# Performance work log

Hardware: AMD Instinct MI355X
Metric: run time of the kernel (lower is better)

Reference implementation:

```python
import jax, jax.numpy as jnp
import numpy as np
import math

B, S, D, NH, L = 4, 1024, 512, 8, 2
PRED, COUT = 96, 512
DH = D // NH
EPS_BACKEND = 1e-6
EPS_LN = 1e-5


def setup_inputs() -> dict:
    key = jax.random.key(0)
    ks = jax.random.split(key, 8)
    return {
        "x_enc": jax.random.normal(ks[0], (B, S, D), jnp.float32),
        "x_mark_enc": jax.random.normal(ks[1], (B, S, 4), jnp.float32),
        "x_dec": jax.random.normal(ks[2], (B, PRED, D), jnp.float32),
        "x_mark_dec": jax.random.normal(ks[3], (B, PRED, 4), jnp.float32),
        # per-layer mLSTM cell params (stacked over L layers)
        "W_ig": jax.random.normal(ks[4], (L, NH, 3 * D), jnp.float32) * 0.02,
        "b_ig": jnp.zeros((L, NH), jnp.float32),
        "W_fg": jax.random.normal(ks[5], (L, NH, 3 * D), jnp.float32) * 0.02,
        "b_fg": jnp.zeros((L, NH), jnp.float32),
        "ln_w": jnp.ones((L, D), jnp.float32),
        # final head
        "fc_W": jax.random.normal(ks[6], (COUT, D), jnp.float32) * 0.02,
        "fc_b": jnp.zeros((COUT,), jnp.float32),
    }


def _mlstm_cell(q, k, v, W_ig, b_ig, W_fg, b_fg, ln_w):
    """xlstm parallel_stabilized_simple backend + MultiHeadLayerNorm."""
    Bq, Sq, Dq = q.shape
    gate_in = jnp.concatenate([q, k, v], axis=-1)          # [B,S,3D]
    ig = jnp.einsum('bsd,hd->bhs', gate_in, W_ig) + b_ig[None, :, None]  # [B,NH,S]
    fg = jnp.einsum('bsd,hd->bhs', gate_in, W_fg) + b_fg[None, :, None]  # [B,NH,S]

    qh = q.reshape(Bq, Sq, NH, DH).transpose(0, 2, 1, 3)   # [B,NH,S,DH]
    kh = k.reshape(Bq, Sq, NH, DH).transpose(0, 2, 1, 3)
    vh = v.reshape(Bq, Sq, NH, DH).transpose(0, 2, 1, 3)

    log_f = jax.nn.log_sigmoid(fg)                          # [B,NH,S]
    fcum = jnp.cumsum(log_f, axis=-1)                       # F[i] = sum_{t<=i} log_f[t]
    # log_fg_matrix[i,j] = F[i] - F[j] for j<=i, else -inf
    lfg = fcum[..., :, None] - fcum[..., None, :]           # [B,NH,S,S]
    causal = jnp.tril(jnp.ones((Sq, Sq), dtype=bool))
    log_D = jnp.where(causal, lfg + ig[..., None, :], -jnp.inf)  # [B,NH,S,S]

    max_log_D = jnp.max(log_D, axis=-1, keepdims=True)      # row-wise stabilizer
    Dm = jnp.exp(log_D - max_log_D)

    qk = jnp.einsum('bhsd,bhtd->bhst', qh, kh) * (1.0 / math.sqrt(DH))
    C = qk * Dm
    normalizer = jnp.maximum(jnp.abs(jnp.sum(C, axis=-1, keepdims=True)),
                             jnp.exp(-max_log_D))
    Cn = C / (normalizer + EPS_BACKEND)
    h = jnp.einsum('bhst,bhtd->bhsd', Cn, vh)               # [B,NH,S,DH]

    # MultiHeadLayerNorm == GroupNorm over DH per head, weight only (no bias)
    mu = jnp.mean(h, axis=-1, keepdims=True)
    var = jnp.var(h, axis=-1, keepdims=True)
    hn = (h - mu) * jax.lax.rsqrt(var + EPS_LN)
    hn = hn * ln_w.reshape(NH, DH)[None, :, None, :]
    return hn.transpose(0, 2, 1, 3).reshape(Bq, Sq, Dq)     # [B,S,D]


def reference(x_enc, x_mark_enc, x_dec, x_mark_dec,
              W_ig, b_ig, W_fg, b_fg, ln_w, fc_W, fc_b):
    q = x_enc
    k = x_enc
    v = x_enc
    for l in range(L):
        q = _mlstm_cell(q, k, v, W_ig[l], b_ig[l], W_fg[l], b_fg[l], ln_w[l])
    dec_out = jnp.einsum('bsd,od->bso', q[:, -PRED:, :], fc_W) + fc_b
    return dec_out
```

## Files before the change

### kernel.cpp

```cpp
#include <hip/hip_runtime.h>
#include <hip/hip_bf16.h>
#include <math.h>
#include <stdint.h>

#define B_ 4
#define S_ 1024
#define D_ 512
#define NH_ 8
#define DH_ 64
#define L_ 2
#define PRED_ 96
#define COUT_ 512

typedef __attribute__((ext_vector_type(8))) short short8;
typedef __attribute__((ext_vector_type(4))) float f32x4;

__device__ __forceinline__ unsigned short f2bf(float f) {
  union { float f; unsigned int u; } v; v.f = f;
  unsigned int r = v.u + 0x7fffu + ((v.u >> 16) & 1u);
  return (unsigned short)(r >> 16);
}
__device__ __forceinline__ float bf2f(unsigned short h) {
  union { unsigned int u; float f; } v; v.u = (unsigned int)h << 16;
  return v.f;
}

__global__ __launch_bounds__(64) void convkv_kernel(
    const float* __restrict__ x, unsigned short* __restrict__ hiA,
    unsigned short* __restrict__ loA) {
  int bs = blockIdx.x;
  int b = bs >> 10, s = bs & 1023;
  int t = threadIdx.x;
  int h = t >> 3, dh0 = (t & 7) * 8;
  const float* src = x + (size_t)bs * D_ + t * 8;
  float4 v0 = *(const float4*)(src);
  float4 v1 = *(const float4*)(src + 4);
  float xv[8] = {v0.x, v0.y, v0.z, v0.w, v1.x, v1.y, v1.z, v1.w};
  unsigned short hh[8], ll[8];
#pragma unroll
  for (int k = 0; k < 8; ++k) {
    hh[k] = f2bf(xv[k]);
    ll[k] = f2bf(xv[k] - bf2f(hh[k]));
  }
  size_t off = (((size_t)(b * NH_ + h)) * S_ + s) * 64 + dh0;
  *(uint4*)(hiA + off) = *(const uint4*)hh;
  *(uint4*)(loA + off) = *(const uint4*)ll;
}

__global__ __launch_bounds__(256) void transpose_kernel(
    const unsigned short* __restrict__ src_a, unsigned short* __restrict__ dst_a) {
  int jt = blockIdx.x, h = blockIdx.y, b = blockIdx.z;
  int bh = b * NH_ + h, j0 = jt * 64;
  __shared__ unsigned short tile[64][72];
  int t = threadIdx.x;
  {
    int j = t >> 2, dseg = (t & 3) * 16;
    const unsigned short* src = src_a + ((size_t)bh * S_ + j0 + j) * 64 + dseg;
    uint4 a0 = *(const uint4*)(src);
    uint4 a1 = *(const uint4*)(src + 8);
    *(uint4*)(&tile[j][dseg]) = a0;
    *(uint4*)(&tile[j][dseg + 8]) = a1;
  }
  __syncthreads();
  {
    int d = t >> 2, jseg = (t & 3) * 16;
    unsigned short us[16];
#pragma unroll
    for (int k = 0; k < 16; ++k) us[k] = tile[jseg + k][d];
    unsigned short* dst = dst_a + ((size_t)bh * 64 + d) * S_ + j0 + jseg;
    *(uint4*)(dst) = *(const uint4*)us;
    *(uint4*)(dst + 8) = *(const uint4*)(us + 8);
  }
}

__global__ __launch_bounds__(256) void gates2_kernel(
    const float* __restrict__ q, const float* __restrict__ x,
    const float* __restrict__ Wig, const float* __restrict__ big,
    const float* __restrict__ Wfg, const float* __restrict__ bfg,
    float* __restrict__ ig_out, float* __restrict__ fg_out) {
  int sc = blockIdx.x, hg = blockIdx.y, b = blockIdx.z;
  __shared__ float Wq_s[8][512];
  __shared__ float Wc_s[8][512];
  for (int idx = threadIdx.x; idx < 8 * 512; idx += 256) {
    int p = idx >> 9, e = idx & 511;
    int h = hg * 4 + (p >> 1);
    const float* Wr = ((p & 1) ? Wfg : Wig) + (size_t)h * (3 * D_);
    Wq_s[p][e] = Wr[e];
    Wc_s[p][e] = Wr[512 + e] + Wr[1024 + e];
  }
  __syncthreads();
  int wv = threadIdx.x >> 6, l = threadIdx.x & 63;
  for (int rr = 0; rr < 8; ++rr) {
    int s = sc * 32 + wv * 8 + rr;
    const float* qrow = q + ((size_t)(b * S_ + s)) * D_;
    const float* xrow = x + ((size_t)(b * S_ + s)) * D_;
    float ql[8], xl[8];
#pragma unroll
    for (int k = 0; k < 8; ++k) { ql[k] = qrow[l + 64 * k]; xl[k] = xrow[l + 64 * k]; }
#pragma unroll
    for (int p = 0; p < 8; ++p) {
      float acc = 0.f;
#pragma unroll
      for (int k = 0; k < 8; ++k)
        acc += Wq_s[p][l + 64 * k] * ql[k] + Wc_s[p][l + 64 * k] * xl[k];
#pragma unroll
      for (int off = 32; off; off >>= 1) acc += __shfl_down(acc, off);
      if (l == 0) {
        int h = hg * 4 + (p >> 1);
        float v = acc + ((p & 1) ? bfg : big)[h];
        ((p & 1) ? fg_out : ig_out)[((size_t)(b * NH_ + h)) * S_ + s] = v;
      }
    }
  }
}

__global__ __launch_bounds__(64) void scan_kernel(
    const float* __restrict__ ig, const float* __restrict__ fg,
    float* __restrict__ a_out, float* __restrict__ amax_out) {
  int bh = blockIdx.x;
  int lane = threadIdx.x;
  const float* igr = ig + (size_t)bh * S_;
  const float* fgr = fg + (size_t)bh * S_;
  const int CH = S_ / 64;
  float lf[16], av[16];
  float lsum = 0.f;
  int base = lane * CH;
  for (int u = 0; u < CH; ++u) {
    float xv = fgr[base + u];
    float ls = (xv >= 0.f) ? -log1pf(__expf(-xv)) : (xv - log1pf(__expf(xv)));
    lf[u] = ls; lsum += ls;
  }
  float pref = lsum;
#pragma unroll
  for (int off = 1; off < 64; off <<= 1) {
    float t = __shfl_up(pref, off);
    if (lane >= off) pref += t;
  }
  float F = pref - lsum;
  float lamax = -INFINITY;
  for (int u = 0; u < CH; ++u) {
    F += lf[u];
    float a = igr[base + u] - F;
    av[u] = a;
    lamax = fmaxf(lamax, a);
  }
  float pmax = lamax;
#pragma unroll
  for (int off = 1; off < 64; off <<= 1) {
    float t = __shfl_up(pmax, off);
    if (lane >= off) pmax = fmaxf(pmax, t);
  }
  float run = __shfl_up(pmax, 1);
  if (lane == 0) run = -INFINITY;
  for (int u = 0; u < CH; ++u) {
    run = fmaxf(run, av[u]);
    size_t o = (size_t)bh * S_ + base + u;
    a_out[o] = av[u];
    amax_out[o] = run;
  }
}

__global__ __launch_bounds__(256) void attn_mfma_kernel(
    const float* __restrict__ qin,
    const unsigned short* __restrict__ kH, const unsigned short* __restrict__ kL,
    const unsigned short* __restrict__ tH, const unsigned short* __restrict__ tL,
    const float* __restrict__ a_arr, const float* __restrict__ amax_arr,
    const float* __restrict__ lnw, float* __restrict__ out,
    unsigned short* __restrict__ outH, unsigned short* __restrict__ outL,
    int write_bf, int it0, int orow0, int out_srows) {
  int it = blockIdx.x + it0, h = blockIdx.y, b = blockIdx.z;
  int i0 = it * 64;
  int bh = b * NH_ + h;
  int tid = threadIdx.x;
  int w = tid >> 6, l = tid & 63;
  int l15 = l & 15, lg = l >> 4;

  __shared__ __align__(16) unsigned char smem[49152 + 256];
  unsigned char* KsH = smem;
  unsigned char* KsL = smem + 8192;
  unsigned char* VtH = smem + 16384;
  unsigned char* VtL = smem + 24576;
  unsigned char* PwH = smem + 32768 + w * 2048;
  unsigned char* PwL = smem + 40960 + w * 2048;
  float* aLds = (float*)(smem + 49152);

  short8 qh[2], qlo[2];
  {
    const float* qrow = qin + ((size_t)(b * S_ + i0 + w * 16 + l15)) * D_ + h * DH_;
#pragma unroll
    for (int ks = 0; ks < 2; ++ks) {
      const float* p = qrow + ks * 32 + lg * 8;
      float4 v0 = *(const float4*)(p);
      float4 v1 = *(const float4*)(p + 4);
      float xv[8] = {v0.x, v0.y, v0.z, v0.w, v1.x, v1.y, v1.z, v1.w};
      unsigned short hh[8], ll[8];
#pragma unroll
      for (int k = 0; k < 8; ++k) {
        hh[k] = f2bf(xv[k]);
        ll[k] = f2bf(xv[k] - bf2f(hh[k]));
      }
      qh[ks] = *(const short8*)hh;
      qlo[ks] = *(const short8*)ll;
    }
  }
  float am_i = amax_arr[(size_t)bh * S_ + i0 + w * 16 + l15];
  const float* abase = a_arr + (size_t)bh * S_;

  f32x4 acc[4];
#pragma unroll
  for (int nt = 0; nt < 4; ++nt) acc[nt] = (f32x4){0.f, 0.f, 0.f, 0.f};

  const unsigned short* KsrcH = kH + (size_t)bh * S_ * 64;
  const unsigned short* KsrcL = kL + (size_t)bh * S_ * 64;
  const unsigned short* TsrcH = tH + (size_t)bh * 64 * S_;
  const unsigned short* TsrcL = tL + (size_t)bh * 64 * S_;

  for (int jt = 0; jt <= it; ++jt) {
    int j0 = jt * 64;
    __syncthreads();
    {
      int r = w * 16 + l15;
#pragma unroll
      for (int gb = 0; gb < 8; gb += 4) {
        int g = gb + lg;
        int sw = r * 128 + ((g ^ (r & 7)) * 16);
        *(uint4*)(KsH + sw) = *(const uint4*)(KsrcH + ((size_t)(j0 + r)) * 64 + g * 8);
        *(uint4*)(KsL + sw) = *(const uint4*)(KsrcL + ((size_t)(j0 + r)) * 64 + g * 8);
        *(uint4*)(VtH + sw) = *(const uint4*)(TsrcH + (size_t)r * S_ + j0 + g * 8);
        *(uint4*)(VtL + sw) = *(const uint4*)(TsrcL + (size_t)r * S_ + j0 + g * 8);
      }
    }
    if (tid < 64) aLds[tid] = abase[j0 + tid];
    __syncthreads();
    int i_g = i0 + w * 16 + l15;
#pragma unroll
    for (int js = 0; js < 4; ++js) {
      f32x4 st = (f32x4){0.f, 0.f, 0.f, 0.f};
      int krow = js * 16 + l15;
      int key = krow & 7;
      short8 kh0 = *(const short8*)(KsH + krow * 128 + (((0 + lg) ^ key) * 16));
      short8 kh1 = *(const short8*)(KsH + krow * 128 + (((4 + lg) ^ key) * 16));
      short8 kl0 = *(const short8*)(KsL + krow * 128 + (((0 + lg) ^ key) * 16));
      short8 kl1 = *(const short8*)(KsL + krow * 128 + (((4 + lg) ^ key) * 16));
      st = __builtin_amdgcn_mfma_f32_16x16x32_bf16(kh0, qh[0], st, 0, 0, 0);
      st = __builtin_amdgcn_mfma_f32_16x16x32_bf16(kh1, qh[1], st, 0, 0, 0);
      st = __builtin_amdgcn_mfma_f32_16x16x32_bf16(kh0, qlo[0], st, 0, 0, 0);
      st = __builtin_amdgcn_mfma_f32_16x16x32_bf16(kh1, qlo[1], st, 0, 0, 0);
      st = __builtin_amdgcn_mfma_f32_16x16x32_bf16(kl0, qh[0], st, 0, 0, 0);
      st = __builtin_amdgcn_mfma_f32_16x16x32_bf16(kl1, qh[1], st, 0, 0, 0);
      int jb_loc = js * 16 + lg * 4;
      unsigned int pkh[2], pkl[2];
#pragma unroll
      for (int r2 = 0; r2 < 2; ++r2) {
        unsigned int ph = 0, pl = 0;
#pragma unroll
        for (int rr = 0; rr < 2; ++rr) {
          int r = r2 * 2 + rr;
          int jl = jb_loc + r;
          float e = __expf(fminf(aLds[jl] - am_i, 0.f));
          float wv = (j0 + jl <= i_g) ? st[r] * 0.125f * e : 0.f;
          unsigned short whi = f2bf(wv);
          unsigned short wlo = f2bf(wv - bf2f(whi));
          ph |= (unsigned int)whi << (rr * 16);
          pl |= (unsigned int)wlo << (rr * 16);
        }
        pkh[r2] = ph; pkl[r2] = pl;
      }
      int g = js * 2 + (lg >> 1);
      int pw_off = l15 * 128 + ((g ^ (l15 & 7)) * 16) + (lg & 1) * 8;
      *(uint2*)(PwH + pw_off) = make_uint2(pkh[0], pkh[1]);
      *(uint2*)(PwL + pw_off) = make_uint2(pkl[0], pkl[1]);
    }
#pragma unroll
    for (int ks = 0; ks < 2; ++ks) {
      int pg = ((ks * 4 + lg) ^ (l15 & 7)) * 16;
      short8 ph = *(const short8*)(PwH + l15 * 128 + pg);
      short8 pl = *(const short8*)(PwL + l15 * 128 + pg);
#pragma unroll
      for (int nt = 0; nt < 4; ++nt) {
        int vr = nt * 16 + l15;
        int vg = vr * 128 + (((ks * 4 + lg) ^ (vr & 7)) * 16);
        short8 vh = *(const short8*)(VtH + vg);
        short8 vl = *(const short8*)(VtL + vg);
        acc[nt] = __builtin_amdgcn_mfma_f32_16x16x32_bf16(ph, vh, acc[nt], 0, 0, 0);
        acc[nt] = __builtin_amdgcn_mfma_f32_16x16x32_bf16(pl, vh, acc[nt], 0, 0, 0);
        acc[nt] = __builtin_amdgcn_mfma_f32_16x16x32_bf16(ph, vl, acc[nt], 0, 0, 0);
      }
    }
  }

  float lw[4];
#pragma unroll
  for (int nt = 0; nt < 4; ++nt) lw[nt] = lnw[h * DH_ + nt * 16 + l15];
#pragma unroll
  for (int r = 0; r < 4; ++r) {
    int il = lg * 4 + r;
    int i_glob = i0 + w * 16 + il;
    float hv[4], s1 = 0.f, s2 = 0.f;
#pragma unroll
    for (int nt = 0; nt < 4; ++nt) {
      hv[nt] = acc[nt][r];
      s1 += hv[nt]; s2 += hv[nt] * hv[nt];
    }
#pragma unroll
    for (int off = 1; off < 16; off <<= 1) {
      s1 += __shfl_xor(s1, off); s2 += __shfl_xor(s2, off);
    }
    float mean = s1 * (1.f / 64.f);
    float var = s2 * (1.f / 64.f) - mean * mean;
    float rstd = rsqrtf(var + 1e-5f);
    size_t ro = ((size_t)(b * out_srows + (i_glob - orow0))) * D_ + h * DH_;
    if (!write_bf) {
#pragma unroll
      for (int nt = 0; nt < 4; ++nt)
        out[ro + nt * 16 + l15] = (hv[nt] - mean) * rstd * lw[nt];
    } else {
#pragma unroll
      for (int nt = 0; nt < 4; ++nt) {
        float v = (hv[nt] - mean) * rstd * lw[nt];
        unsigned short hi = f2bf(v);
        outH[ro + nt * 16 + l15] = hi;
        outL[ro + nt * 16 + l15] = f2bf(v - bf2f(hi));
      }
    }
  }
}

__global__ __launch_bounds__(256) void fc3_kernel(
    const unsigned short* __restrict__ qH, const unsigned short* __restrict__ qL,
    const float* __restrict__ W, const float* __restrict__ bias,
    float* __restrict__ out) {
  int rt = blockIdx.x, ot = blockIdx.y;
  int tid = threadIdx.x;
  int w = tid >> 6, l = tid & 63, l15 = l & 15, lg = l >> 4;
  int r_flat = rt * 64 + w * 16 + l15;
  int b = r_flat / 96, pc = r_flat - b * 96;
  const unsigned short* qHrow = qH + ((size_t)(b * 128 + 32 + pc)) * D_;
  const unsigned short* qLrow = qL + ((size_t)(b * 128 + 32 + pc)) * D_;
  int obase = ot * 64;

  f32x4 acc[4];
#pragma unroll
  for (int og = 0; og < 4; ++og) acc[og] = (f32x4){0.f, 0.f, 0.f, 0.f};

#pragma unroll 2
  for (int ks = 0; ks < 16; ++ks) {
    int k0 = ks * 32 + lg * 8;
    short8 ah = *(const short8*)(qHrow + k0);
    short8 al = *(const short8*)(qLrow + k0);
#pragma unroll
    for (int og = 0; og < 4; ++og) {
      const float* wrow = W + (size_t)(obase + og * 16 + l15) * D_ + k0;
      float4 w0 = *(const float4*)(wrow);
      float4 w1 = *(const float4*)(wrow + 4);
      float wv[8] = {w0.x, w0.y, w0.z, w0.w, w1.x, w1.y, w1.z, w1.w};
      unsigned short bhh[8], bll[8];
#pragma unroll
      for (int k = 0; k < 8; ++k) {
        bhh[k] = f2bf(wv[k]);
        bll[k] = f2bf(wv[k] - bf2f(bhh[k]));
      }
      short8 bh = *(const short8*)bhh;
      short8 bl = *(const short8*)bll;
      acc[og] = __builtin_amdgcn_mfma_f32_16x16x32_bf16(ah, bh, acc[og], 0, 0, 0);
      acc[og] = __builtin_amdgcn_mfma_f32_16x16x32_bf16(al, bh, acc[og], 0, 0, 0);
      acc[og] = __builtin_amdgcn_mfma_f32_16x16x32_bf16(ah, bl, acc[og], 0, 0, 0);
    }
  }
  int rbase = rt * 64 + w * 16 + lg * 4;
#pragma unroll
  for (int og = 0; og < 4; ++og) {
    int o = obase + og * 16 + l15;
    float bs = bias[o];
#pragma unroll
    for (int r = 0; r < 4; ++r)
      out[(size_t)(rbase + r) * COUT_ + o] = acc[og][r] + bs;
  }
}

extern "C" void kernel_launch(void* const* d_in, const int* in_sizes, int n_in,
                              void* d_out, int out_size, void* d_ws, size_t ws_size,
                              hipStream_t stream) {
  const float* x_enc = (const float*)d_in[0];
  const float* W_ig = (const float*)d_in[4];
  const float* b_ig = (const float*)d_in[5];
  const float* W_fg = (const float*)d_in[6];
  const float* b_fg = (const float*)d_in[7];
  const float* ln_w = (const float*)d_in[8];
  const float* fc_W = (const float*)d_in[9];
  const float* fc_b = (const float*)d_in[10];

  float* ws = (float*)d_ws;
  const size_t NBSD = (size_t)B_ * S_ * D_;
  const size_t NBHS = (size_t)B_ * NH_ * S_;
  float* h1 = ws;
  float* ig = h1 + NBSD;
  float* fg = ig + NBHS;
  float* aA = fg + NBHS;
  float* amaxA = aA + NBHS;
  unsigned short* kvhH = (unsigned short*)(amaxA + NBHS);
  unsigned short* kvhL = kvhH + NBSD;
  unsigned short* kvTH = kvhL + NBSD;
  unsigned short* kvTL = kvTH + NBSD;
  unsigned short* hqH = kvTL + NBSD;
  unsigned short* hqL = hqH + (size_t)B_ * 128 * D_;

  convkv_kernel<<<B_ * S_, 64, 0, stream>>>(x_enc, kvhH, kvhL);
  transpose_kernel<<<dim3(S_ / 64, NH_, B_), 256, 0, stream>>>(kvhH, kvTH);
  transpose_kernel<<<dim3(S_ / 64, NH_, B_), 256, 0, stream>>>(kvhL, kvTL);

  for (int l = 0; l < L_; ++l) {
    const float* qin = (l == 0) ? x_enc : h1;
    gates2_kernel<<<dim3(S_ / 32, 2, B_), 256, 0, stream>>>(
        qin, x_enc,
        W_ig + (size_t)l * NH_ * 3 * D_, b_ig + (size_t)l * NH_,
        W_fg + (size_t)l * NH_ * 3 * D_, b_fg + (size_t)l * NH_, ig, fg);
    scan_kernel<<<B_ * NH_, 64, 0, stream>>>(ig, fg, aA, amaxA);
    if (l == 0) {
      attn_mfma_kernel<<<dim3(S_ / 64, NH_, B_), 256, 0, stream>>>(
          qin, kvhH, kvhL, kvTH, kvTL, aA, amaxA, ln_w + (size_t)l * D_,
          h1, (unsigned short*)nullptr, (unsigned short*)nullptr, 0, 0, 0, S_);
    } else {
      attn_mfma_kernel<<<dim3(2, NH_, B_), 256, 0, stream>>>(
          qin, kvhH, kvhL, kvTH, kvTL, aA, amaxA, ln_w + (size_t)l * D_,
          (float*)nullptr, hqH, hqL, 1, 14, 896, 128);
    }
  }
  fc3_kernel<<<dim3(6, 8), 256, 0, stream>>>(hqH, hqL, fc_W, fc_b, (float*)d_out);
}
```

Baseline: 299.0 us.

## Give each wave its own 16-row tile, pair causal tiles, read K/V from global

The attention kernel is restructured so each wavefront independently owns a 16-row query tile, and in layer 0 processes a complementary pair (t and 63-t) to balance causal work. K and V tiles are no longer staged in shared LDS with block barriers; each wave loads its MFMA operands straight from global memory and relies on the cache. Block-to-(b,h) mapping is permuted so blocks sharing a head land on the same XCD for L2 reuse. This removes __syncthreads and the causal load imbalance, at the cost of more global/cache traffic and less data sharing across waves.

```diff
diff --git a/kernel.cpp b/kernel.cpp
--- a/kernel.cpp
+++ b/kernel.cpp
@@ -160,169 +160,182 @@
   }
 }
 
-__global__ __launch_bounds__(256) void attn_mfma_kernel(
+__device__ __forceinline__ void attn_tile_proc(
+    int t, int b, int h, int bh, int l15, int lg,
+    const float* __restrict__ qin,
+    const unsigned short* __restrict__ KsrcH, const unsigned short* __restrict__ KsrcL,
+    const unsigned short* __restrict__ TsrcH, const unsigned short* __restrict__ TsrcL,
+    const float* __restrict__ abase, const float* __restrict__ amax_arr,
+    const float* __restrict__ lnw,
+    float* __restrict__ out, unsigned short* __restrict__ outH,
+    unsigned short* __restrict__ outL,
+    int write_bf, int orow0, int out_srows,
+    unsigned char* PwH, unsigned char* PwL) {
+  int i0 = t * 16;
+  short8 qh[2], qlo[2];
+  {
+    const float* qrow = qin + ((size_t)(b * S_ + i0 + l15)) * D_ + h * DH_;
+#pragma unroll
+    for (int ks = 0; ks < 2; ++ks) {
+      const float* p = qrow + ks * 32 + lg * 8;
+      float4 v0 = *(const float4*)(p);
+      float4 v1 = *(const float4*)(p + 4);
+      float xv[8] = {v0.x, v0.y, v0.z, v0.w, v1.x, v1.y, v1.z, v1.w};
+      unsigned short hh[8], ll[8];
+#pragma unroll
+      for (int k = 0; k < 8; ++k) {
+        hh[k] = f2bf(xv[k]);
+        ll[k] = f2bf(xv[k] - bf2f(hh[k]));
+      }
+      qh[ks] = *(const short8*)hh;
+      qlo[ks] = *(const short8*)ll;
+    }
+  }
+  float am_i = amax_arr[(size_t)bh * S_ + i0 + l15];
+  int i_g = i0 + l15;
+  f32x4 acc[4];
+#pragma unroll
+  for (int nt = 0; nt < 4; ++nt) acc[nt] = (f32x4){0.f, 0.f, 0.f, 0.f};
+
+  int jt_max = (i0 + 15) >> 6;
+  for (int jt = 0; jt <= jt_max; ++jt) {
+    int j0 = jt * 64;
+#pragma unroll
+    for (int js = 0; js < 4; ++js) {
+      int jr = j0 + js * 16 + l15;
+      const unsigned short* kp = KsrcH + (size_t)jr * 64 + lg * 8;
+      const unsigned short* kpl = KsrcL + (size_t)jr * 64 + lg * 8;
+      short8 kh0 = *(const short8*)(kp);
+      short8 kh1 = *(const short8*)(kp + 32);
+      short8 kl0 = *(const short8*)(kpl);
+      short8 kl1 = *(const short8*)(kpl + 32);
+      f32x4 st = (f32x4){0.f, 0.f, 0.f, 0.f};
+      st = __builtin_amdgcn_mfma_f32_16x16x32_bf16(kh0, qh[0], st, 0, 0, 0);
+      st = __builtin_amdgcn_mfma_f32_16x16x32_bf16(kh1, qh[1], st, 0, 0, 0);
+      st = __builtin_amdgcn_mfma_f32_16x16x32_bf16(kh0, qlo[0], st, 0, 0, 0);
+      st = __builtin_amdgcn_mfma_f32_16x16x32_bf16(kh1, qlo[1], st, 0, 0, 0);
+      st = __builtin_amdgcn_mfma_f32_16x16x32_bf16(kl0, qh[0], st, 0, 0, 0);
+      st = __builtin_amdgcn_mfma_f32_16x16x32_bf16(kl1, qh[1], st, 0, 0, 0);
+      int jb = js * 16 + lg * 4;
+      unsigned int pkh[2], pkl[2];
+#pragma unroll
+      for (int r2 = 0; r2 < 2; ++r2) {
+        unsigned int ph = 0, pl = 0;
+#pragma unroll
+        for (int rr = 0; rr < 2; ++rr) {
+          int r = r2 * 2 + rr;
+          int jl = jb + r;
+          float e = __expf(fminf(abase[j0 + jl] - am_i, 0.f));
+          float wv = (j0 + jl <= i_g) ? st[r] * 0.125f * e : 0.f;
+          unsigned short whi = f2bf(wv);
+          ph |= (unsigned int)whi << (rr * 16);
+          pl |= (unsigned int)f2bf(wv - bf2f(whi)) << (rr * 16);
+        }
+        pkh[r2] = ph; pkl[r2] = pl;
+      }
+      int g = js * 2 + (lg >> 1);
+      int pw_off = l15 * 128 + ((g ^ (l15 & 7)) * 16) + (lg & 1) * 8;
+      *(uint2*)(PwH + pw_off) = make_uint2(pkh[0], pkh[1]);
+      *(uint2*)(PwL + pw_off) = make_uint2(pkl[0], pkl[1]);
+    }
+#pragma unroll
+    for (int ks = 0; ks < 2; ++ks) {
+      int pg = ((ks * 4 + lg) ^ (l15 & 7)) * 16;
+      short8 ph = *(const short8*)(PwH + l15 * 128 + pg);
+      short8 pl = *(const short8*)(PwL + l15 * 128 + pg);
+#pragma unroll
+      for (int nt = 0; nt < 4; ++nt) {
+        const unsigned short* vp = TsrcH + (size_t)(nt * 16 + l15) * S_ + j0 + (ks * 4 + lg) * 8;
+        const unsigned short* vpl = TsrcL + (size_t)(nt * 16 + l15) * S_ + j0 + (ks * 4 + lg) * 8;
+        short8 vh = *(const short8*)vp;
+        short8 vl = *(const short8*)vpl;
+        acc[nt] = __builtin_amdgcn_mfma_f32_16x16x32_bf16(ph, vh, acc[nt], 0, 0, 0);
+        acc[nt] = __builtin_amdgcn_mfma_f32_16x16x32_bf16(pl, vh, acc[nt], 0, 0, 0);
+        acc[nt] = __builtin_amdgcn_mfma_f32_16x16x32_bf16(ph, vl, acc[nt], 0, 0, 0);
+      }
+    }
+  }
+
+  float lw[4];
+#pragma unroll
+  for (int nt = 0; nt < 4; ++nt) lw[nt] = lnw[h * DH_ + nt * 16 + l15];
+#pragma unroll
+  for (int r = 0; r < 4; ++r) {
+    int i_glob = i0 + lg * 4 + r;
+    float hv[4], s1 = 0.f, s2 = 0.f;
+#pragma unroll
+    for (int nt = 0; nt < 4; ++nt) {
+      hv[nt] = acc[nt][r];
+      s1 += hv[nt]; s2 += hv[nt] * hv[nt];
+    }
+#pragma unroll
+    for (int off = 1; off < 16; off <<= 1) {
+      s1 += __shfl_xor(s1, off); s2 += __shfl_xor(s2, off);
+    }
+    float mean = s1 * (1.f / 64.f);
+    float var = s2 * (1.f / 64.f) - mean * mean;
+    float rstd = rsqrtf(var + 1e-5f);
+    size_t ro = ((size_t)(b * out_srows + (i_glob - orow0))) * D_ + h * DH_;
+    if (!write_bf) {
+#pragma unroll
+      for (int nt = 0; nt < 4; ++nt)
+        out[ro + nt * 16 + l15] = (hv[nt] - mean) * rstd * lw[nt];
+    } else {
+#pragma unroll
+      for (int nt = 0; nt < 4; ++nt) {
+        float v = (hv[nt] - mean) * rstd * lw[nt];
+        unsigned short hi = f2bf(v);
+        outH[ro + nt * 16 + l15] = hi;
+        outL[ro + nt * 16 + l15] = f2bf(v - bf2f(hi));
+      }
+    }
+  }
+}
+
+__global__ __launch_bounds__(256) void attn_wave_kernel(
     const float* __restrict__ qin,
     const unsigned short* __restrict__ kH, const unsigned short* __restrict__ kL,
     const unsigned short* __restrict__ tH, const unsigned short* __restrict__ tL,
     const float* __restrict__ a_arr, const float* __restrict__ amax_arr,
     const float* __restrict__ lnw, float* __restrict__ out,
     unsigned short* __restrict__ outH, unsigned short* __restrict__ outL,
-    int write_bf, int it0, int orow0, int out_srows) {
-  int it = blockIdx.x + it0, h = blockIdx.y, b = blockIdx.z;
-  int i0 = it * 64;
-  int bh = b * NH_ + h;
+    int write_bf, int mode, int orow0, int out_srows) {
   int tid = threadIdx.x;
   int w = tid >> 6, l = tid & 63;
   int l15 = l & 15, lg = l >> 4;
-
-  __shared__ __align__(16) unsigned char smem[49152 + 256];
-  unsigned char* KsH = smem;
-  unsigned char* KsL = smem + 8192;
-  unsigned char* VtH = smem + 16384;
-  unsigned char* VtL = smem + 24576;
-  unsigned char* PwH = smem + 32768 + w * 2048;
-  unsigned char* PwL = smem + 40960 + w * 2048;
-  float* aLds = (float*)(smem + 49152);
-
-  short8 qh[2], qlo[2];
-  {
-    const float* qrow = qin + ((size_t)(b * S_ + i0 + w * 16 + l15)) * D_ + h * DH_;
-#pragma unroll
-    for (int ks = 0; ks < 2; ++ks) {
-      const float* p = qrow + ks * 32 + lg * 8;
-      float4 v0 = *(const float4*)(p);
-      float4 v1 = *(const float4*)(p + 4);
-      float xv[8] = {v0.x, v0.y, v0.z, v0.w, v1.x, v1.y, v1.z, v1.w};
-      unsigned short hh[8], ll[8];
-#pragma unroll
-      for (int k = 0; k < 8; ++k) {
-        hh[k] = f2bf(xv[k]);
-        ll[k] = f2bf(xv[k] - bf2f(hh[k]));
-      }
-      qh[ks] = *(const short8*)hh;
-      qlo[ks] = *(const short8*)ll;
-    }
-  }
-  float am_i = amax_arr[(size_t)bh * S_ + i0 + w * 16 + l15];
-  const float* abase = a_arr + (size_t)bh * S_;
-
-  f32x4 acc[4];
-#pragma unroll
-  for (int nt = 0; nt < 4; ++nt) acc[nt] = (f32x4){0.f, 0.f, 0.f, 0.f};
-
+  __shared__ __align__(16) unsigned char smem[16384];
+  unsigned char* PwH = smem + w * 4096;
+  unsigned char* PwL = PwH + 2048;
+
+  int b, h, pi;
+  if (mode == 0) {
+    int f = blockIdx.x + 8 * (blockIdx.y + 8 * blockIdx.z);
+    int xcd = f & 7, s = f >> 3;
+    int bh = xcd * 4 + (s & 3);
+    b = bh >> 3; h = bh & 7;
+    pi = (s >> 2) * 4 + w;
+  } else {
+    int f = blockIdx.x + 2 * (blockIdx.y + 8 * blockIdx.z);
+    int xcd = f & 7, s = f >> 3;
+    int bh = xcd * 4 + (s & 3);
+    b = bh >> 3; h = bh & 7;
+    pi = (s >> 2) * 4 + w;
+  }
+  int bh = b * NH_ + h;
   const unsigned short* KsrcH = kH + (size_t)bh * S_ * 64;
   const unsigned short* KsrcL = kL + (size_t)bh * S_ * 64;
   const unsigned short* TsrcH = tH + (size_t)bh * 64 * S_;
   const unsigned short* TsrcL = tL + (size_t)bh * 64 * S_;
-
-  for (int jt = 0; jt <= it; ++jt) {
-    int j0 = jt * 64;
-    __syncthreads();
-    {
-      int r = w * 16 + l15;
-#pragma unroll
-      for (int gb = 0; gb < 8; gb += 4) {
-        int g = gb + lg;
-        int sw = r * 128 + ((g ^ (r & 7)) * 16);
-        *(uint4*)(KsH + sw) = *(const uint4*)(KsrcH + ((size_t)(j0 + r)) * 64 + g * 8);
-        *(uint4*)(KsL + sw) = *(const uint4*)(KsrcL + ((size_t)(j0 + r)) * 64 + g * 8);
-        *(uint4*)(VtH + sw) = *(const uint4*)(TsrcH + (size_t)r * S_ + j0 + g * 8);
-        *(uint4*)(VtL + sw) = *(const uint4*)(TsrcL + (size_t)r * S_ + j0 + g * 8);
-      }
-    }
-    if (tid < 64) aLds[tid] = abase[j0 + tid];
-    __syncthreads();
-    int i_g = i0 + w * 16 + l15;
-#pragma unroll
-    for (int js = 0; js < 4; ++js) {
-      f32x4 st = (f32x4){0.f, 0.f, 0.f, 0.f};
-      int krow = js * 16 + l15;
-      int key = krow & 7;
-      short8 kh0 = *(const short8*)(KsH + krow * 128 + (((0 + lg) ^ key) * 16));
-      short8 kh1 = *(const short8*)(KsH + krow * 128 + (((4 + lg) ^ key) * 16));
-      short8 kl0 = *(const short8*)(KsL + krow * 128 + (((0 + lg) ^ key) * 16));
-      short8 kl1 = *(const short8*)(KsL + krow * 128 + (((4 + lg) ^ key) * 16));
-      st = __builtin_amdgcn_mfma_f32_16x16x32_bf16(kh0, qh[0], st, 0, 0, 0);
-      st = __builtin_amdgcn_mfma_f32_16x16x32_bf16(kh1, qh[1], st, 0, 0, 0);
-      st = __builtin_amdgcn_mfma_f32_16x16x32_bf16(kh0, qlo[0], st, 0, 0, 0);
-      st = __builtin_amdgcn_mfma_f32_16x16x32_bf16(kh1, qlo[1], st, 0, 0, 0);
-      st = __builtin_amdgcn_mfma_f32_16x16x32_bf16(kl0, qh[0], st, 0, 0, 0);
-      st = __builtin_amdgcn_mfma_f32_16x16x32_bf16(kl1, qh[1], st, 0, 0, 0);
-      int jb_loc = js * 16 + lg * 4;
-      unsigned int pkh[2], pkl[2];
-#pragma unroll
-      for (int r2 = 0; r2 < 2; ++r2) {
-        unsigned int ph = 0, pl = 0;
-#pragma unroll
-        for (int rr = 0; rr < 2; ++rr) {
-          int r = r2 * 2 + rr;
-          int jl = jb_loc + r;
-          float e = __expf(fminf(aLds[jl] - am_i, 0.f));
-          float wv = (j0 + jl <= i_g) ? st[r] * 0.125f * e : 0.f;
-          unsigned short whi = f2bf(wv);
-          unsigned short wlo = f2bf(wv - bf2f(whi));
-          ph |= (unsigned int)whi << (rr * 16);
-          pl |= (unsigned int)wlo << (rr * 16);
-        }
-        pkh[r2] = ph; pkl[r2] = pl;
-      }
-      int g = js * 2 + (lg >> 1);
-      int pw_off = l15 * 128 + ((g ^ (l15 & 7)) * 16) + (lg & 1) * 8;
-      *(uint2*)(PwH + pw_off) = make_uint2(pkh[0], pkh[1]);
-      *(uint2*)(PwL + pw_off) = make_uint2(pkl[0], pkl[1]);
-    }
-#pragma unroll
-    for (int ks = 0; ks < 2; ++ks) {
-      int pg = ((ks * 4 + lg) ^ (l15 & 7)) * 16;
-      short8 ph = *(const short8*)(PwH + l15 * 128 + pg);
-      short8 pl = *(const short8*)(PwL + l15 * 128 + pg);
-#pragma unroll
-      for (int nt = 0; nt < 4; ++nt) {
-        int vr = nt * 16 + l15;
-        int vg = vr * 128 + (((ks * 4 + lg) ^ (vr & 7)) * 16);
-        short8 vh = *(const short8*)(VtH + vg);
-        short8 vl = *(const short8*)(VtL + vg);
-        acc[nt] = __builtin_amdgcn_mfma_f32_16x16x32_bf16(ph, vh, acc[nt], 0, 0, 0);
-        acc[nt] = __builtin_amdgcn_mfma_f32_16x16x32_bf16(pl, vh, acc[nt], 0, 0, 0);
-        acc[nt] = __builtin_amdgcn_mfma_f32_16x16x32_bf16(ph, vl, acc[nt], 0, 0, 0);
-      }
-    }
-  }
-
-  float lw[4];
-#pragma unroll
-  for (int nt = 0; nt < 4; ++nt) lw[nt] = lnw[h * DH_ + nt * 16 + l15];
-#pragma unroll
-  for (int r = 0; r < 4; ++r) {
-    int il = lg * 4 + r;
-    int i_glob = i0 + w * 16 + il;
-    float hv[4], s1 = 0.f, s2 = 0.f;
-#pragma unroll
-    for (int nt = 0; nt < 4; ++nt) {
-      hv[nt] = acc[nt][r];
-      s1 += hv[nt]; s2 += hv[nt] * hv[nt];
-    }
-#pragma unroll
-    for (int off = 1; off < 16; off <<= 1) {
-      s1 += __shfl_xor(s1, off); s2 += __shfl_xor(s2, off);
-    }
-    float mean = s1 * (1.f / 64.f);
-    float var = s2 * (1.f / 64.f) - mean * mean;
-    float rstd = rsqrtf(var + 1e-5f);
-    size_t ro = ((size_t)(b * out_srows + (i_glob - orow0))) * D_ + h * DH_;
-    if (!write_bf) {
-#pragma unroll
-      for (int nt = 0; nt < 4; ++nt)
-        out[ro + nt * 16 + l15] = (hv[nt] - mean) * rstd * lw[nt];
-    } else {
-#pragma unroll
-      for (int nt = 0; nt < 4; ++nt) {
-        float v = (hv[nt] - mean) * rstd * lw[nt];
-        unsigned short hi = f2bf(v);
-        outH[ro + nt * 16 + l15] = hi;
-        outL[ro + nt * 16 + l15] = f2bf(v - bf2f(hi));
-      }
-    }
+  const float* abase = a_arr + (size_t)bh * S_;
+
+  int tA = (mode == 0) ? pi : (56 + pi);
+  attn_tile_proc(tA, b, h, bh, l15, lg, qin, KsrcH, KsrcL, TsrcH, TsrcL,
+                 abase, amax_arr, lnw, out, outH, outL,
+                 write_bf, orow0, out_srows, PwH, PwL);
+  if (mode == 0) {
+    attn_tile_proc(63 - pi, b, h, bh, l15, lg, qin, KsrcH, KsrcL, TsrcH, TsrcL,
+                   abase, amax_arr, lnw, out, outH, outL,
+                   write_bf, orow0, out_srows, PwH, PwL);
   }
 }
 
@@ -417,13 +430,13 @@
         W_fg + (size_t)l * NH_ * 3 * D_, b_fg + (size_t)l * NH_, ig, fg);
     scan_kernel<<<B_ * NH_, 64, 0, stream>>>(ig, fg, aA, amaxA);
     if (l == 0) {
-      attn_mfma_kernel<<<dim3(S_ / 64, NH_, B_), 256, 0, stream>>>(
+      attn_wave_kernel<<<dim3(8, NH_, B_), 256, 0, stream>>>(
           qin, kvhH, kvhL, kvTH, kvTL, aA, amaxA, ln_w + (size_t)l * D_,
           h1, (unsigned short*)nullptr, (unsigned short*)nullptr, 0, 0, 0, S_);
     } else {
-      attn_mfma_kernel<<<dim3(2, NH_, B_), 256, 0, stream>>>(
+      attn_wave_kernel<<<dim3(2, NH_, B_), 256, 0, stream>>>(
           qin, kvhH, kvhL, kvTH, kvTL, aA, amaxA, ln_w + (size_t)l * D_,
-          (float*)nullptr, hqH, hqL, 1, 14, 896, 128);
+          (float*)nullptr, hqH, hqL, 1, 1, 896, 128);
     }
   }
   fc3_kernel<<<dim3(6, 8), 256, 0, stream>>>(hqH, hqL, fc_W, fc_b, (float*)d_out);
```

After: 382.6 us. 27.9% more time.
